# Optimization experiments

Measured on AMD Instinct MI355X. Metric: run time of the kernel, lower is better.

## Reference

```python
import jax, jax.numpy as jnp
import numpy as np

R_MAX = 32
S_MAX = 2
C_Z = 128
IN_DIM = 4 * R_MAX + 2 * S_MAX + 7  # 139
B, N = 1, 1024


def setup_inputs() -> dict:
    key = jax.random.key(0)
    ks = jax.random.split(key, 6)
    asym_id = jnp.sort(jax.random.randint(ks[0], (B, N), 0, 4), axis=-1)
    residue_index = jnp.sort(jax.random.randint(ks[1], (B, N), 0, 512), axis=-1)
    entity_id = jnp.sort(jax.random.randint(ks[2], (B, N), 0, 3), axis=-1)
    sym_id = jax.random.randint(ks[3], (B, N), 0, 3)
    token_index = jnp.sort(jax.random.randint(ks[4], (B, N), 0, 1024), axis=-1)
    W = jax.random.normal(ks[5], (IN_DIM, C_Z), dtype=jnp.float32) * 0.02
    return {"asym_id": asym_id, "residue_index": residue_index,
            "entity_id": entity_id, "sym_id": sym_id,
            "token_index": token_index, "W": W}


def reference(asym_id, residue_index, entity_id, sym_id, token_index, W):
    # Pairwise same-chain / same-residue / same-entity masks: [B, N, N]
    same_chain = asym_id[..., :, None] == asym_id[..., None, :]
    same_res = residue_index[..., :, None] == residue_index[..., None, :]
    same_ent = entity_id[..., :, None] == entity_id[..., None, :]

    # Clipped relative indices (values in [0, 2*r_max+1] / [0, 2*s_max+1])
    d_res = jnp.where(
        same_chain,
        jnp.clip(residue_index[..., :, None] - residue_index[..., None, :] + R_MAX, 0, 2 * R_MAX),
        2 * R_MAX + 1)
    d_tok = jnp.where(
        same_chain & same_res,
        jnp.clip(token_index[..., :, None] - token_index[..., None, :] + R_MAX, 0, 2 * R_MAX),
        2 * R_MAX + 1)
    d_chain = jnp.where(
        same_ent,
        jnp.clip(sym_id[..., :, None] - sym_id[..., None, :] + S_MAX, 0, 2 * S_MAX),
        2 * S_MAX + 1)

    # concat(one_hot(d_res,66), one_hot(d_tok,66), same_ent, one_hot(d_chain,6)) @ W
    # == sum of gathered weight rows: avoids materializing the [B,N,N,139] one-hot.
    n_pos = 2 * (R_MAX + 1)          # 66
    W_pos = W[:n_pos]                # rows 0..65
    W_tok = W[n_pos:2 * n_pos]       # rows 66..131
    w_ent = W[2 * n_pos]             # row 132
    W_chn = W[2 * n_pos + 1:]        # rows 133..138

    p = (W_pos[d_res] + W_tok[d_tok]
         + same_ent[..., None].astype(W.dtype) * w_ent
         + W_chn[d_chain])           # [B, N, N, c_z]
    return p
```

## Files before the change

### kernel.cpp

```cpp
#include <hip/hip_runtime.h>


typedef float f4 __attribute__((ext_vector_type(4)));

constexpr int kN  = 1024;
constexpr int kSplit = 2;

__global__ __launch_bounds__(256) void relpos_kernel(
    const int* __restrict__ asym,
    const int* __restrict__ resi,
    const int* __restrict__ ent,
    const int* __restrict__ sym,
    const int* __restrict__ tok,
    const float* __restrict__ W,
    float* __restrict__ out)
{
    const int tid = threadIdx.x;
    const int c4  = tid & 31;
    const int jg  = tid >> 5;

    const int i     = blockIdx.x / kSplit;
    const int jbase = (blockIdx.x % kSplit) * (kN / kSplit);

    const int ai = asym[i];
    const int ri = resi[i];
    const int ei = ent[i];
    const int si = sym[i];
    const int ti = tok[i];

    const f4* __restrict__ W4 = reinterpret_cast<const f4*>(W);
    f4* __restrict__ out4     = reinterpret_cast<f4*>(out);

    const f4 went = W4[132 * 32 + c4];

    for (int jj = 0; jj < kN / kSplit; jj += 8) {
        const int j  = jbase + jj + jg;
        const int aj = asym[j];
        const int rj = resi[j];
        const int ej = ent[j];
        const int sj = sym[j];
        const int tj = tok[j];

        const bool same_chain = (ai == aj);
        const bool same_res   = (ri == rj);
        const bool same_ent   = (ei == ej);

        int dres = min(max(ri - rj + 32, 0), 64);
        if (!same_chain) dres = 65;
        int dtok = min(max(ti - tj + 32, 0), 64);
        if (!(same_chain && same_res)) dtok = 65;
        int dchn = min(max(si - sj + 2, 0), 4);
        if (!same_ent) dchn = 5;

        const f4 wa = W4[dres * 32 + c4];
        const f4 wb = W4[(66 + dtok) * 32 + c4];
        const f4 wc = W4[(133 + dchn) * 32 + c4];

        f4 v = wa + wb + wc;
        if (same_ent) v += went;

        __builtin_nontemporal_store(v, &out4[(size_t)(i * kN + j) * 32 + c4]);
    }
}

extern "C" void kernel_launch(void* const* d_in, const int* in_sizes, int n_in,
                              void* d_out, int out_size, void* d_ws, size_t ws_size,
                              hipStream_t stream) {
    const int*   asym = (const int*)d_in[0];
    const int*   resi = (const int*)d_in[1];
    const int*   ent  = (const int*)d_in[2];
    const int*   sym  = (const int*)d_in[3];
    const int*   tok  = (const int*)d_in[4];
    const float* W    = (const float*)d_in[5];
    float*       out  = (float*)d_out;

    dim3 grid(kN * kSplit);
    dim3 block(256);
    relpos_kernel<<<grid, block, 0, stream>>>(asym, resi, ent, sym, tok, W, out);
}
```

Baseline: 113.2 us.

## Stage weight table and packed j-keys in LDS, fold entity row into chain rows

```diff
diff --git a/kernel.cpp b/kernel.cpp
--- a/kernel.cpp
+++ b/kernel.cpp
@@ -3,10 +3,11 @@
 
 typedef float f4 __attribute__((ext_vector_type(4)));
 
-constexpr int kN  = 1024;
-constexpr int kSplit = 2;
+constexpr int kN     = 1024;
+constexpr int kRowF4 = 32;
+constexpr int kWF4   = 139 * kRowF4;
 
-__global__ __launch_bounds__(256) void relpos_kernel(
+__global__ __launch_bounds__(1024) void relpos_kernel(
     const int* __restrict__ asym,
     const int* __restrict__ resi,
     const int* __restrict__ ent,
@@ -15,51 +16,61 @@
     const float* __restrict__ W,
     float* __restrict__ out)
 {
+    __shared__ f4  sW[kWF4];
+    __shared__ int sKey[kN];
+
     const int tid = threadIdx.x;
-    const int c4  = tid & 31;
-    const int jg  = tid >> 5;
+    const f4* __restrict__ W4 = reinterpret_cast<const f4*>(W);
 
-    const int i     = blockIdx.x / kSplit;
-    const int jbase = (blockIdx.x % kSplit) * (kN / kSplit);
+    for (int idx = tid; idx < kWF4; idx += 1024) {
+        f4 v = W4[idx];
+        if (idx >= 133 * kRowF4 && idx < 138 * kRowF4)
+            v += W4[132 * kRowF4 + (idx & (kRowF4 - 1))];
+        sW[idx] = v;
+    }
+    {
+        const int j = tid;
+        sKey[j] = (asym[j] & 3) | ((ent[j] & 3) << 2) | ((sym[j] & 3) << 4)
+                | ((resi[j] & 511) << 6) | ((tok[j] & 1023) << 15);
+    }
+    __syncthreads();
 
-    const int ai = asym[i];
-    const int ri = resi[i];
-    const int ei = ent[i];
-    const int si = sym[i];
-    const int ti = tok[i];
+    const int c4 = tid & 31;
+    const int jg = tid >> 5;
 
-    const f4* __restrict__ W4 = reinterpret_cast<const f4*>(W);
-    f4* __restrict__ out4     = reinterpret_cast<f4*>(out);
+    f4* __restrict__ out4 = reinterpret_cast<f4*>(out);
 
-    const f4 went = W4[132 * 32 + c4];
+    const int i0 = blockIdx.x * 2;
+    for (int ii = 0; ii < 2; ++ii) {
+        const int i = i0 + ii;
+        const int ai = asym[i], ri = resi[i], ei = ent[i], si = sym[i], ti = tok[i];
+        f4* __restrict__ orow = out4 + (size_t)i * kN * kRowF4 + c4;
 
-    for (int jj = 0; jj < kN / kSplit; jj += 8) {
-        const int j  = jbase + jj + jg;
-        const int aj = asym[j];
-        const int rj = resi[j];
-        const int ej = ent[j];
-        const int sj = sym[j];
-        const int tj = tok[j];
+        for (int it = 0; it < kN / 32; ++it) {
+            const int j = it * 32 + jg;
+            const int k = sKey[j];
+            const int aj =  k        & 3;
+            const int ej = (k >> 2)  & 3;
+            const int sj = (k >> 4)  & 3;
+            const int rj = (k >> 6)  & 511;
+            const int tj = (k >> 15) & 1023;
 
-        const bool same_chain = (ai == aj);
-        const bool same_res   = (ri == rj);
-        const bool same_ent   = (ei == ej);
+            const bool same_chain = (ai == aj);
+            const bool same_ent   = (ei == ej);
 
-        int dres = min(max(ri - rj + 32, 0), 64);
-        if (!same_chain) dres = 65;
-        int dtok = min(max(ti - tj + 32, 0), 64);
-        if (!(same_chain && same_res)) dtok = 65;
-        int dchn = min(max(si - sj + 2, 0), 4);
-        if (!same_ent) dchn = 5;
+            int dres = min(max(ri - rj + 32, 0), 64);
+            if (!same_chain) dres = 65;
+            int dtok = min(max(ti - tj + 32, 0), 64);
+            if (!(same_chain && (ri == rj))) dtok = 65;
+            int dchn = min(max(si - sj + 2, 0), 4);
+            if (!same_ent) dchn = 5;
 
-        const f4 wa = W4[dres * 32 + c4];
-        const f4 wb = W4[(66 + dtok) * 32 + c4];
-        const f4 wc = W4[(133 + dchn) * 32 + c4];
+            const f4 wa = sW[dres * kRowF4 + c4];
+            const f4 wb = sW[(66 + dtok) * kRowF4 + c4];
+            const f4 wc = sW[(133 + dchn) * kRowF4 + c4];
 
-        f4 v = wa + wb + wc;
-        if (same_ent) v += went;
-
-        __builtin_nontemporal_store(v, &out4[(size_t)(i * kN + j) * 32 + c4]);
+            __builtin_nontemporal_store(wa + wb + wc, &orow[(size_t)j * kRowF4]);
+        }
     }
 }
 
@@ -74,7 +85,5 @@
     const float* W    = (const float*)d_in[5];
     float*       out  = (float*)d_out;
 
-    dim3 grid(kN * kSplit);
-    dim3 block(256);
-    relpos_kernel<<<grid, block, 0, stream>>>(asym, resi, ent, sym, tok, W, out);
+    relpos_kernel<<<dim3(kN / 2), dim3(1024), 0, stream>>>(asym, resi, ent, sym, tok, W, out);
 }
```

Result: faster. 103.9 us (-8.2%).
